# Kernel optimization log

Hardware: AMD Instinct MI355X
Metric: run time of the kernel (lower is better)

The kernel has to match this reference:

```python
import jax, jax.numpy as jnp
import numpy as np

N, E, G = 100000, 300000, 4096
ND, ED, H, ZI, ZS, NE, L = 64, 16, 256, 128, 128, 8, 3
LAMBDA_GRL = 1.0


def setup_inputs() -> dict:
    key = jax.random.key(0)
    ks = iter(jax.random.split(key, 64))
    def nrm(shape, scale=0.05):
        return jax.random.normal(next(ks), shape, jnp.float32) * scale
    inp = {
        'x': jax.random.normal(next(ks), (N, ND), jnp.float32),
        'edge_index': jax.random.randint(next(ks), (2, E), 0, N),
        'edge_attr': jax.random.normal(next(ks), (E, ED), jnp.float32),
        'batch': jnp.sort(jax.random.randint(next(ks), (N,), 0, G)),
        'node_W': nrm((ND, H)), 'node_b': nrm((H,)),
        'conv_eps': jnp.zeros((L,), jnp.float32),
        'edge_W': nrm((L, ED, H)), 'edge_b': nrm((L, H)),
        'mlp_W1': nrm((L, H, H)), 'mlp_b1': nrm((L, H)),
        'mlp_W2': nrm((L, H, H)), 'mlp_b2': nrm((L, H)),
        'gn_w': jnp.ones((L, H), jnp.float32), 'gn_b': jnp.zeros((L, H), jnp.float32),
        'gn_ms': jnp.ones((L, H), jnp.float32),
        'finv_W1': nrm((H, ZI)), 'finv_b1': nrm((ZI,)),
        'finv_W2': nrm((ZI, ZI)), 'finv_b2': nrm((ZI,)),
        'fspu_W1': nrm((H, ZS)), 'fspu_b1': nrm((ZS,)),
        'fspu_W2': nrm((ZS, ZS)), 'fspu_b2': nrm((ZS,)),
        'pred_W1': nrm((ZI, ZI)), 'pred_b1': nrm((ZI,)),
        'pred_W2': nrm((ZI, 1)), 'pred_b2': nrm((1,)),
        'adv_W1': nrm((ZI, ZI)), 'adv_b1': nrm((ZI,)),
        'adv_W2': nrm((ZI, NE)), 'adv_b2': nrm((NE,)),
    }
    return inp


def _mlp2(h, W1, b1, W2, b2):
    return jax.nn.relu(h @ W1 + b1) @ W2 + b2


def reference(x, edge_index, edge_attr, batch, node_W, node_b, conv_eps,
              edge_W, edge_b, mlp_W1, mlp_b1, mlp_W2, mlp_b2,
              gn_w, gn_b, gn_ms,
              finv_W1, finv_b1, finv_W2, finv_b2,
              fspu_W1, fspu_b1, fspu_W2, fspu_b2,
              pred_W1, pred_b1, pred_W2, pred_b2,
              adv_W1, adv_b1, adv_W2, adv_b2):
    src, dst = edge_index[0], edge_index[1]
    cnt = jax.ops.segment_sum(jnp.ones((N, 1), jnp.float32), batch, num_segments=G)
    cnt = jnp.maximum(cnt, 1.0)
    h = x @ node_W + node_b  # [N,H]
    for l in range(L):
        # GINEConv: sum_j relu(x_j + lin(e_ij))
        e = edge_attr @ edge_W[l] + edge_b[l]            # [E,H]
        m = jax.nn.relu(h[src] + e)                      # [E,H]
        agg = jax.ops.segment_sum(m, dst, num_segments=N)
        h = _mlp2((1.0 + conv_eps[l]) * h + agg, mlp_W1[l], mlp_b1[l], mlp_W2[l], mlp_b2[l])
        # GraphNorm
        mean = jax.ops.segment_sum(h, batch, num_segments=G) / cnt  # [G,H]
        out = h - gn_ms[l] * mean[batch]
        var = jax.ops.segment_sum(out * out, batch, num_segments=G) / cnt
        h = out * jax.lax.rsqrt(var[batch] + 1e-5) * gn_w[l] + gn_b[l]
        h = jax.nn.relu(h)  # dropout is identity at eval
    hg = jax.ops.segment_sum(h, batch, num_segments=G) / cnt  # global_mean_pool [G,H]
    z_inv = _mlp2(hg, finv_W1, finv_b1, finv_W2, finv_b2)
    z_spu = _mlp2(hg, fspu_W1, fspu_b1, fspu_W2, fspu_b2)
    yhat = _mlp2(z_inv, pred_W1, pred_b1, pred_W2, pred_b2)[:, 0]
    # gradient reversal: identity fwd, -lambda on bwd
    grl = jax.lax.stop_gradient(z_inv) * (1.0 + LAMBDA_GRL) - LAMBDA_GRL * z_inv
    envhat = _mlp2(grl, adv_W1, adv_b1, adv_W2, adv_b2)
    return (hg, z_inv, z_spu, yhat, envhat)
```

## Files before the change

### kernel.cpp

```cpp
#include <hip/hip_runtime.h>
#include <hip/hip_bf16.h>

typedef __bf16 bf16_t;
typedef __bf16 bf16x8 __attribute__((ext_vector_type(8)));
typedef __bf16 bf16x4 __attribute__((ext_vector_type(4)));
typedef float  f32x4  __attribute__((ext_vector_type(4)));

static constexpr int N_NODES = 100000;
static constexpr int N_EDGES = 300000;
static constexpr int N_GRAPH = 4096;
static constexpr int H  = 256;
static constexpr int ND = 64;
static constexpr int ZIC = 128;
static constexpr int NE = 8;
static constexpr int SCAN_B = 1024;

__device__ __forceinline__ int clampi(int v, int lo, int hi) {
  return v < lo ? lo : (v > hi ? hi : v);
}

__device__ __forceinline__ void dma16(const bf16_t* g, bf16_t* lds_base) {
  __builtin_amdgcn_global_load_lds(
      (const __attribute__((address_space(1))) void*)g,
      (__attribute__((address_space(3))) void*)lds_base, 16, 0, 0);
}

__global__ void compute_starts_kernel(const int* __restrict__ batch,
                                      int* __restrict__ starts,
                                      int* __restrict__ counts,
                                      int* __restrict__ cursor, int N, int G) {
  int i = blockIdx.x * blockDim.x + threadIdx.x;
  if (i >= N) return;
  counts[i] = 0;
  cursor[i] = 0;
  int b = clampi(batch[i], 0, G - 1);
  if (i == 0) {
    for (int g = 0; g <= b; ++g) starts[g] = 0;
  } else {
    int p = clampi(batch[i - 1], 0, G - 1);
    for (int g = p + 1; g <= b; ++g) starts[g] = i;
  }
  if (i == N - 1) {
    for (int g = b + 1; g <= G; ++g) starts[g] = N;
  }
}

__global__ void count_deg_kernel(const int* __restrict__ dst, int* __restrict__ counts, int E, int N) {
  int e = blockIdx.x * blockDim.x + threadIdx.x;
  if (e < E) atomicAdd(&counts[clampi(dst[e], 0, N - 1)], 1);
}

__global__ __launch_bounds__(SCAN_B) void scan1_kernel(const int* __restrict__ counts,
                                                       int* __restrict__ offs,
                                                       int* __restrict__ bsum, int N) {
  __shared__ int tmp[SCAN_B];
  int i = blockIdx.x * SCAN_B + threadIdx.x;
  int v = (i < N) ? counts[i] : 0;
  tmp[threadIdx.x] = v;
  __syncthreads();
  for (int d = 1; d < SCAN_B; d <<= 1) {
    int t = (threadIdx.x >= d) ? tmp[threadIdx.x - d] : 0;
    __syncthreads();
    tmp[threadIdx.x] += t;
    __syncthreads();
  }
  if (i < N) offs[i + 1] = tmp[threadIdx.x];
  if (threadIdx.x == SCAN_B - 1) bsum[blockIdx.x] = tmp[SCAN_B - 1];
  if (i == 0) offs[0] = 0;
}

__global__ void scan2_kernel(int* __restrict__ bsum, int nblk) {
  if (blockIdx.x == 0 && threadIdx.x == 0) {
    int run = 0;
    for (int b = 0; b < nblk; ++b) { int v = bsum[b]; bsum[b] = run; run += v; }
  }
}

__global__ __launch_bounds__(SCAN_B) void scan3_kernel(int* __restrict__ offs,
                                                       const int* __restrict__ bsum, int N) {
  int i = blockIdx.x * SCAN_B + threadIdx.x;
  if (i < N) offs[i + 1] += bsum[blockIdx.x];
}

__global__ void fill_scatter_kernel(const int* __restrict__ src, const int* __restrict__ dst,
                                    const float* __restrict__ eattr,
                                    const int* __restrict__ offs, int* __restrict__ cursor,
                                    int* __restrict__ src_srt, bf16_t* __restrict__ eat16,
                                    int E, int N) {
  int e = blockIdx.x * blockDim.x + threadIdx.x;
  if (e >= E) return;
  int d = clampi(dst[e], 0, N - 1);
  int pos = offs[d] + atomicAdd(&cursor[d], 1);
  if ((unsigned)pos >= (unsigned)E) return;
  int s = src[e];
  src_srt[pos] = ((unsigned)s < (unsigned)N_NODES) ? s : 0;
  const float* ea = eattr + (size_t)e * 16;
  union { bf16_t b[16]; uint4 u[2]; } pk;
#pragma unroll
  for (int k = 0; k < 16; ++k) pk.b[k] = (bf16_t)ea[k];
  uint4* dst16 = (uint4*)(eat16 + ((size_t)pos << 4));
  dst16[0] = pk.u[0];
  dst16[1] = pk.u[1];
}

__global__ void build_ewt16_kernel(const float* __restrict__ edge_W,
                                   bf16_t* __restrict__ ewt) {
  int idx = blockIdx.x * blockDim.x + threadIdx.x;
  if (idx >= 3 * 256 * 16) return;
  int l = idx / (256 * 16);
  int rem = idx - l * 256 * 16;
  int n = rem >> 4, k = rem & 15;
  ewt[idx] = (bf16_t)edge_W[(size_t)l * 16 * 256 + k * 256 + n];
}

__global__ void transpose_kernel(const float* __restrict__ W,
                                 bf16_t* __restrict__ Wt, int K, int Nc,
                                 size_t srcStride, size_t dstStride) {
  __shared__ float tile[32][33];
  const float* Wz = W + (size_t)blockIdx.z * srcStride;
  bf16_t* Wtz = Wt + (size_t)blockIdx.z * dstStride;
  int n0 = blockIdx.x * 32, k0 = blockIdx.y * 32;
  int tx = threadIdx.x, ty = threadIdx.y;
  for (int i = ty; i < 32; i += 8)
    tile[i][tx] = Wz[(size_t)(k0 + i) * Nc + n0 + tx];
  __syncthreads();
  for (int i = ty; i < 32; i += 8)
    Wtz[(size_t)(n0 + i) * K + k0 + tx] = (bf16_t)tile[tx][i];
}

__device__ __forceinline__ void load8_to_lds(const bf16_t* p, bool valid, uint4* dst) {
  uint4 v = make_uint4(0u, 0u, 0u, 0u);
  if (valid) v = *(const uint4*)p;
  *dst = v;
}
__device__ __forceinline__ void load8_to_lds(const float* p, bool valid, uint4* dst) {
  float4 f0 = make_float4(0.f, 0.f, 0.f, 0.f), f1 = f0;
  if (valid) { f0 = *(const float4*)p; f1 = *(const float4*)(p + 4); }
  union { bf16_t b[8]; uint4 u; } pk;
  pk.b[0] = (bf16_t)f0.x; pk.b[1] = (bf16_t)f0.y;
  pk.b[2] = (bf16_t)f0.z; pk.b[3] = (bf16_t)f0.w;
  pk.b[4] = (bf16_t)f1.x; pk.b[5] = (bf16_t)f1.y;
  pk.b[6] = (bf16_t)f1.z; pk.b[7] = (bf16_t)f1.w;
  *dst = pk.u;
}

template<int K, bool RELU, bool OUTF32, typename TIN>
__global__ __launch_bounds__(256) void gemm128_kernel(
    const TIN* __restrict__ U, const bf16_t* __restrict__ Wt,
    const float* __restrict__ bias, void* __restrict__ Out, int M, int Nc) {
  constexpr int LDT = 72;
  __shared__ bf16_t Ut[128 * LDT];
  __shared__ bf16_t Wl[128 * LDT];
  const int m0 = blockIdx.x * 128;
  const int n0 = blockIdx.y * 128;
  const int t = threadIdx.x;
  const int lane = t & 63;
  const int wave = t >> 6;
  const int wm = (wave >> 1) * 64;
  const int wn = (wave & 1) * 64;
  const int srow = t >> 1;
  const int sk = (t & 1) * 32;
  const int lr = lane & 15;
  const int lq = lane >> 4;
  const bool aok = (m0 + srow) < M;
  f32x4 acc[4][4] = {};

  for (int k0 = 0; k0 < K; k0 += 64) {
    const TIN* up = U + (size_t)(m0 + srow) * K + k0 + sk;
    const bf16_t* wp = Wt + (size_t)(n0 + srow) * K + k0 + sk;
#pragma unroll
    for (int q = 0; q < 4; ++q) {
      load8_to_lds(up + q * 8, aok, (uint4*)&Ut[srow * LDT + sk + q * 8]);
      load8_to_lds(wp + q * 8, true, (uint4*)&Wl[srow * LDT + sk + q * 8]);
    }
    __syncthreads();
#pragma unroll
    for (int s = 0; s < 2; ++s) {
      bf16x8 a[4], b[4];
#pragma unroll
      for (int mt = 0; mt < 4; ++mt)
        a[mt] = *(const bf16x8*)(&Ut[(wm + mt * 16 + lr) * LDT + s * 32 + lq * 8]);
#pragma unroll
      for (int nt = 0; nt < 4; ++nt)
        b[nt] = *(const bf16x8*)(&Wl[(wn + nt * 16 + lr) * LDT + s * 32 + lq * 8]);
#pragma unroll
      for (int mt = 0; mt < 4; ++mt)
#pragma unroll
        for (int nt = 0; nt < 4; ++nt)
          acc[mt][nt] = __builtin_amdgcn_mfma_f32_16x16x32_bf16(
              a[mt], b[nt], acc[mt][nt], 0, 0, 0);
    }
    __syncthreads();
  }

#pragma unroll
  for (int mt = 0; mt < 4; ++mt)
#pragma unroll
    for (int nt = 0; nt < 4; ++nt) {
      int col = n0 + wn + nt * 16 + lr;
      float bcol = bias[col];
#pragma unroll
      for (int r = 0; r < 4; ++r) {
        int row = m0 + wm + mt * 16 + lq * 4 + r;
        if (row < M) {
          float vv = acc[mt][nt][r] + bcol;
          if (RELU) vv = vv > 0.f ? vv : 0.f;
          if (OUTF32) ((float*)Out)[(size_t)row * Nc + col] = vv;
          else        ((bf16_t*)Out)[(size_t)row * Nc + col] = (bf16_t)vv;
        }
      }
    }
}

template<int K, bool RELU>
__global__ __launch_bounds__(512) void gemm256_dma_kernel(
    const bf16_t* __restrict__ U, const bf16_t* __restrict__ Wt,
    const float* __restrict__ bias, bf16_t* __restrict__ Out, int M) {
  __shared__ bf16_t Ut[128 * 64];
  __shared__ bf16_t Wl[256 * 64];
  const int t = threadIdx.x;
  const int lane = t & 63;
  const int wave = t >> 6;
  const int m0 = blockIdx.x * 128;
  const int wm = (wave >> 2) * 64;
  const int wn = (wave & 3) * 64;
  const int lr = lane & 15;
  const int lq = lane >> 4;
  const int subrow = lane >> 3;
  const int lchunk = (lane & 7) ^ subrow;
  f32x4 acc[4][4] = {};

  for (int k0 = 0; k0 < K; k0 += 64) {
#pragma unroll
    for (int c = 0; c < 2; ++c) {
      int urow = m0 + c * 64 + wave * 8 + subrow;
      if (urow >= M) urow = M - 1;
      dma16(U + (size_t)urow * K + k0 + lchunk * 8, &Ut[(c * 64 + wave * 8) * 64]);
    }
#pragma unroll
    for (int c = 0; c < 4; ++c) {
      int wrow = c * 64 + wave * 8 + subrow;
      dma16(Wt + (size_t)wrow * K + k0 + lchunk * 8, &Wl[(c * 64 + wave * 8) * 64]);
    }
    __syncthreads();
#pragma unroll
    for (int s = 0; s < 2; ++s) {
      bf16x8 a[4], b[4];
#pragma unroll
      for (int mt = 0; mt < 4; ++mt)
        a[mt] = *(const bf16x8*)(&Ut[(wm + mt * 16 + lr) * 64 + (((s * 4 + lq) ^ (lr & 7)) << 3)]);
#pragma unroll
      for (int nt = 0; nt < 4; ++nt)
        b[nt] = *(const bf16x8*)(&Wl[(wn + nt * 16 + lr) * 64 + (((s * 4 + lq) ^ (lr & 7)) << 3)]);
#pragma unroll
      for (int mt = 0; mt < 4; ++mt)
#pragma unroll
        for (int nt = 0; nt < 4; ++nt)
          acc[mt][nt] = __builtin_amdgcn_mfma_f32_16x16x32_bf16(
              a[mt], b[nt], acc[mt][nt], 0, 0, 0);
    }
    __syncthreads();
  }

#pragma unroll
  for (int mt = 0; mt < 4; ++mt)
#pragma unroll
    for (int nt = 0; nt < 4; ++nt) {
      int col = wn + nt * 16 + lr;
      float bcol = bias[col];
#pragma unroll
      for (int r = 0; r < 4; ++r) {
        int row = m0 + wm + mt * 16 + lq * 4 + r;
        if (row < M) {
          float vv = acc[mt][nt][r] + bcol;
          if (RELU) vv = vv > 0.f ? vv : 0.f;
          Out[(size_t)row * H + col] = (bf16_t)vv;
        }
      }
    }
}

__global__ __launch_bounds__(256) void gine_gather_mfma_kernel(
    const bf16_t* __restrict__ h, const bf16_t* __restrict__ eat16,
    const int* __restrict__ src_sorted, const int* __restrict__ offs,
    const bf16_t* __restrict__ ewt, const float* __restrict__ eb,
    const float* __restrict__ eps_p, bf16_t* __restrict__ u) {
  constexpr int HP = H + 8;
  __shared__ bf16_t slin[2][16 * HP];
  const int t = threadIdx.x;
  const int wave = t >> 6;
  const int lane = t & 63;
  const int lr = lane & 15;
  const int lq = lane >> 4;
  const int lane4 = lane * 4;
  const int n0 = blockIdx.x * 4;
  const int nodeN = n0 + wave;

  bf16x4 hs = *(const bf16x4*)(h + (size_t)nodeN * H + lane4);

  bf16x8 bfrag[4];
#pragma unroll
  for (int nt = 0; nt < 4; ++nt) {
    bf16x8 bv = {};
    if (lq < 2)
      bv = *(const bf16x8*)(ewt + ((wave * 64 + nt * 16 + lr) << 4) + (lq << 3));
    bfrag[nt] = bv;
  }
  float ebv[4];
#pragma unroll
  for (int i = 0; i < 4; ++i) ebv[i] = eb[lane4 + i];

  int bs = offs[n0], be = offs[n0 + 4];
  bs = clampi(bs, 0, N_EDGES);
  be = clampi(be, bs, N_EDGES);
  int ns = offs[nodeN], ne = offs[nodeN + 1];
  ns = clampi(ns, bs, be);
  ne = clampi(ne, ns, be);

  float acc[4] = {0.f, 0.f, 0.f, 0.f};
  int parity = 0;

  for (int cb = bs; cb < be; cb += 16, parity ^= 1) {
    int arow = cb + lr;
    if (arow >= N_EDGES) arow = N_EDGES - 1;
    bf16x8 afrag = {};
    if (lq < 2)
      afrag = *(const bf16x8*)(eat16 + ((size_t)arow << 4) + (lq << 3));

    int j0 = ns > cb ? ns : cb;
    int j1 = ne < cb + 16 ? ne : cb + 16;
    int sidx[4];
    bf16x4 hv[4];
    if (j0 < j1) {
#pragma unroll
      for (int q = 0; q < 4; ++q) {
        int jj = j0 + q; if (jj > j1 - 1) jj = j1 - 1;
        sidx[q] = src_sorted[jj];
      }
    }

    f32x4 c[4];
#pragma unroll
    for (int nt = 0; nt < 4; ++nt) {
      f32x4 z = {};
      c[nt] = __builtin_amdgcn_mfma_f32_16x16x32_bf16(afrag, bfrag[nt], z, 0, 0, 0);
    }
#pragma unroll
    for (int nt = 0; nt < 4; ++nt)
#pragma unroll
      for (int r = 0; r < 4; ++r)
        slin[parity][(lq * 4 + r) * HP + wave * 64 + nt * 16 + lr] = (bf16_t)c[nt][r];

    if (j0 < j1) {
#pragma unroll
      for (int q = 0; q < 4; ++q)
        hv[q] = *(const bf16x4*)(h + (size_t)sidx[q] * H + lane4);
    }

    __syncthreads();

    for (int jb = j0; jb < j1; jb += 4) {
      if (jb != j0) {
#pragma unroll
        for (int q = 0; q < 4; ++q) {
          int jj = jb + q; if (jj > j1 - 1) jj = j1 - 1;
          sidx[q] = src_sorted[jj];
        }
#pragma unroll
        for (int q = 0; q < 4; ++q)
          hv[q] = *(const bf16x4*)(h + (size_t)sidx[q] * H + lane4);
      }
#pragma unroll
      for (int q = 0; q < 4; ++q) {
        if (jb + q < j1) {
          bf16x4 lv = *(const bf16x4*)(&slin[parity][(jb + q - cb) * HP + lane4]);
#pragma unroll
          for (int i = 0; i < 4; ++i)
            acc[i] += fmaxf((float)hv[q][i] + (float)lv[i] + ebv[i], 0.f);
        }
      }
    }
  }

  const float sc = 1.0f + eps_p[0];
  union { bf16x4 v; uint2 b; } o;
#pragma unroll
  for (int i = 0; i < 4; ++i) o.v[i] = (bf16_t)(sc * (float)hs[i] + acc[i]);
  *(uint2*)(u + (size_t)nodeN * H + lane4) = o.b;
}

__global__ __launch_bounds__(256) void graphnorm_kernel(
    const bf16_t* __restrict__ v, bf16_t* __restrict__ hout,
    const int* __restrict__ starts,
    const float* __restrict__ w, const float* __restrict__ b,
    const float* __restrict__ ms, float* __restrict__ hg) {
  constexpr int RS = 9;
  constexpr int PS = 13;
  __shared__ float red[4 * 64 * RS];
  __shared__ float prm[64 * PS];
  const int g = blockIdx.x;
  const int t = threadIdx.x;
  const int lane = t & 63;
  const int wave = t >> 6;
  const int c0 = lane * 4;
  int s = starts[g], e = starts[g + 1];
  s = clampi(s, 0, N_NODES);
  e = clampi(e, s, N_NODES);
  const float cnt = (float)((e - s) > 1 ? (e - s) : 1);

  float sx[4] = {0.f, 0.f, 0.f, 0.f}, sxx[4] = {0.f, 0.f, 0.f, 0.f};
  {
    int i = s + wave;
    for (; i + 4 < e; i += 8) {
      bf16x4 x0 = *(const bf16x4*)(v + (size_t)i * H + c0);
      bf16x4 x1 = *(const bf16x4*)(v + (size_t)(i + 4) * H + c0);
#pragma unroll
      for (int j = 0; j < 4; ++j) {
        float f0 = (float)x0[j], f1 = (float)x1[j];
        sx[j] += f0 + f1; sxx[j] += f0 * f0 + f1 * f1;
      }
    }
    if (i < e) {
      bf16x4 x0 = *(const bf16x4*)(v + (size_t)i * H + c0);
#pragma unroll
      for (int j = 0; j < 4; ++j) {
        float f0 = (float)x0[j];
        sx[j] += f0; sxx[j] += f0 * f0;
      }
    }
  }
  float* myred = &red[(wave * 64 + lane) * RS];
#pragma unroll
  for (int j = 0; j < 4; ++j) { myred[j] = sx[j]; myred[4 + j] = sxx[j]; }
  __syncthreads();

  if (wave == 0) {
#pragma unroll
    for (int j = 0; j < 4; ++j) {
      float fsx = red[lane * RS + j] + red[(64 + lane) * RS + j] +
                  red[(128 + lane) * RS + j] + red[(192 + lane) * RS + j];
      float fsxx = red[lane * RS + 4 + j] + red[(64 + lane) * RS + 4 + j] +
                   red[(128 + lane) * RS + 4 + j] + red[(192 + lane) * RS + 4 + j];
      float mean = fsx / cnt;
      float sub = ms[c0 + j] * mean;
      float var = fsxx / cnt - 2.f * sub * mean + sub * sub;
      var = fmaxf(var, 0.f);
      prm[lane * PS + j] = sub;
      prm[lane * PS + 4 + j] = rsqrtf(var + 1e-5f) * w[c0 + j];
      prm[lane * PS + 8 + j] = b[c0 + j];
    }
  }
  __syncthreads();
  float sub[4], inv[4], bb[4];
#pragma unroll
  for (int j = 0; j < 4; ++j) {
    sub[j] = prm[lane * PS + j];
    inv[j] = prm[lane * PS + 4 + j];
    bb[j] = prm[lane * PS + 8 + j];
  }

  float psum[4] = {0.f, 0.f, 0.f, 0.f};
  {
    int i = s + wave;
    for (; i + 4 < e; i += 8) {
      bf16x4 x0 = *(const bf16x4*)(v + (size_t)i * H + c0);
      bf16x4 x1 = *(const bf16x4*)(v + (size_t)(i + 4) * H + c0);
      union { bf16x4 o; uint2 u; } p0, p1;
#pragma unroll
      for (int j = 0; j < 4; ++j) {
        float o0 = ((float)x0[j] - sub[j]) * inv[j] + bb[j];
        float o1 = ((float)x1[j] - sub[j]) * inv[j] + bb[j];
        o0 = o0 > 0.f ? o0 : 0.f;
        o1 = o1 > 0.f ? o1 : 0.f;
        psum[j] += o0 + o1;
        p0.o[j] = (bf16_t)o0; p1.o[j] = (bf16_t)o1;
      }
      *(uint2*)(hout + (size_t)i * H + c0) = p0.u;
      *(uint2*)(hout + (size_t)(i + 4) * H + c0) = p1.u;
    }
    if (i < e) {
      bf16x4 x0 = *(const bf16x4*)(v + (size_t)i * H + c0);
      union { bf16x4 o; uint2 u; } p0;
#pragma unroll
      for (int j = 0; j < 4; ++j) {
        float o0 = ((float)x0[j] - sub[j]) * inv[j] + bb[j];
        o0 = o0 > 0.f ? o0 : 0.f;
        psum[j] += o0;
        p0.o[j] = (bf16_t)o0;
      }
      *(uint2*)(hout + (size_t)i * H + c0) = p0.u;
    }
  }

  if (hg) {
#pragma unroll
    for (int j = 0; j < 4; ++j) myred[j] = psum[j];
    __syncthreads();
    if (wave == 0) {
#pragma unroll
      for (int j = 0; j < 4; ++j) {
        float p = red[lane * RS + j] + red[(64 + lane) * RS + j] +
                  red[(128 + lane) * RS + j] + red[(192 + lane) * RS + j];
        hg[(size_t)g * H + c0 + j] = p / cnt;
      }
    }
  }
}

__global__ __launch_bounds__(256) void heads_fused_kernel(
    const float* __restrict__ hg,
    const bf16_t* __restrict__ fT1, const float* __restrict__ fb1,
    const bf16_t* __restrict__ fT2, const float* __restrict__ fb2,
    const bf16_t* __restrict__ sT1, const float* __restrict__ sb1,
    const bf16_t* __restrict__ sT2, const float* __restrict__ sb2,
    const bf16_t* __restrict__ pT1, const float* __restrict__ pb1,
    const bf16_t* __restrict__ aT1, const float* __restrict__ ab1,
    const float* __restrict__ pW2, const float* __restrict__ pb2,
    const float* __restrict__ aW2, const float* __restrict__ ab2,
    float* __restrict__ out_zi, float* __restrict__ out_zs,
    float* __restrict__ out_yh, float* __restrict__ out_ev) {
  constexpr int LDS_S = 264;
  constexpr int LDZ = 136;
  __shared__ bf16_t BufA[64 * LDS_S];
  __shared__ bf16_t BufB[64 * LDS_S];
  __shared__ bf16_t Z[64 * LDZ];
  const int t = threadIdx.x;
  const int lane = t & 63;
  const int wave = t >> 6;
  const int m0 = blockIdx.x * 64;
  const int lr = lane & 15;
  const int lq = lane >> 4;

  {
    int r = t >> 2, cb = (t & 3) * 64;
    const float* src = hg + (size_t)(m0 + r) * H + cb;
#pragma unroll
    for (int q = 0; q < 8; ++q)
      load8_to_lds(src + q * 8, true, (uint4*)&BufA[r * LDS_S + cb + q * 8]);
  }
  __syncthreads();

  f32x4 acc[4][4];

  {
    const bf16_t* W = (wave < 2) ? fT1 : sT1;
    const float* bb = (wave < 2) ? fb1 : sb1;
    const int wnl = (wave & 1) * 64;
    const int wcol = wave * 64;
#pragma unroll
    for (int mt = 0; mt < 4; ++mt)
#pragma unroll
      for (int nt = 0; nt < 4; ++nt) { f32x4 z = {}; acc[mt][nt] = z; }
    for (int k0 = 0; k0 < 256; k0 += 32) {
      bf16x8 a[4], b[4];
#pragma unroll
      for (int nt = 0; nt < 4; ++nt)
        b[nt] = *(const bf16x8*)(W + (size_t)(wnl + nt * 16 + lr) * 256 + k0 + lq * 8);
#pragma unroll
      for (int mt = 0; mt < 4; ++mt)
        a[mt] = *(const bf16x8*)(&BufA[(mt * 16 + lr) * LDS_S + k0 + lq * 8]);
#pragma unroll
      for (int mt = 0; mt < 4; ++mt)
#pragma unroll
        for (int nt = 0; nt < 4; ++nt)
          acc[mt][nt] = __builtin_amdgcn_mfma_f32_16x16x32_bf16(
              a[mt], b[nt], acc[mt][nt], 0, 0, 0);
    }
    __syncthreads();
#pragma unroll
    for (int nt = 0; nt < 4; ++nt) {
      float bv = bb[wnl + nt * 16 + lr];
      int col = wcol + nt * 16 + lr;
#pragma unroll
      for (int mt = 0; mt < 4; ++mt)
#pragma unroll
        for (int r = 0; r < 4; ++r) {
          int row = mt * 16 + lq * 4 + r;
          float vv = acc[mt][nt][r] + bv;
          BufB[row * LDS_S + col] = (bf16_t)(vv > 0.f ? vv : 0.f);
        }
    }
  }
  __syncthreads();

  {
    const bf16_t* W = (wave < 2) ? fT2 : sT2;
    const float* bb = (wave < 2) ? fb2 : sb2;
    float* outp = (wave < 2) ? out_zi : out_zs;
    const int wnl = (wave & 1) * 64;
    const int kin = (wave < 2) ? 0 : 128;
#pragma unroll
    for (int mt = 0; mt < 4; ++mt)
#pragma unroll
      for (int nt = 0; nt < 4; ++nt) { f32x4 z = {}; acc[mt][nt] = z; }
    for (int k0 = 0; k0 < 128; k0 += 32) {
      bf16x8 a[4], b[4];
#pragma unroll
      for (int nt = 0; nt < 4; ++nt)
        b[nt] = *(const bf16x8*)(W + (size_t)(wnl + nt * 16 + lr) * 128 + k0 + lq * 8);
#pragma unroll
      for (int mt = 0; mt < 4; ++mt)
        a[mt] = *(const bf16x8*)(&BufB[(mt * 16 + lr) * LDS_S + kin + k0 + lq * 8]);
#pragma unroll
      for (int mt = 0; mt < 4; ++mt)
#pragma unroll
        for (int nt = 0; nt < 4; ++nt)
          acc[mt][nt] = __builtin_amdgcn_mfma_f32_16x16x32_bf16(
              a[mt], b[nt], acc[mt][nt], 0, 0, 0);
    }
#pragma unroll
    for (int nt = 0; nt < 4; ++nt) {
      int col = wnl + nt * 16 + lr;
      float bv = bb[col];
#pragma unroll
      for (int mt = 0; mt < 4; ++mt)
#pragma unroll
        for (int r = 0; r < 4; ++r) {
          int row = mt * 16 + lq * 4 + r;
          float vv = acc[mt][nt][r] + bv;
          outp[(size_t)(m0 + row) * ZIC + col] = vv;
          if (wave < 2) Z[row * LDZ + col] = (bf16_t)vv;
        }
    }
  }
  __syncthreads();

  {
    const bf16_t* W = (wave < 2) ? pT1 : aT1;
    const float* bb = (wave < 2) ? pb1 : ab1;
    const int wnl = (wave & 1) * 64;
    const int wcol = wave * 64;
#pragma unroll
    for (int mt = 0; mt < 4; ++mt)
#pragma unroll
      for (int nt = 0; nt < 4; ++nt) { f32x4 z = {}; acc[mt][nt] = z; }
    for (int k0 = 0; k0 < 128; k0 += 32) {
      bf16x8 a[4], b[4];
#pragma unroll
      for (int nt = 0; nt < 4; ++nt)
        b[nt] = *(const bf16x8*)(W + (size_t)(wnl + nt * 16 + lr) * 128 + k0 + lq * 8);
#pragma unroll
      for (int mt = 0; mt < 4; ++mt)
        a[mt] = *(const bf16x8*)(&Z[(mt * 16 + lr) * LDZ + k0 + lq * 8]);
#pragma unroll
      for (int mt = 0; mt < 4; ++mt)
#pragma unroll
        for (int nt = 0; nt < 4; ++nt)
          acc[mt][nt] = __builtin_amdgcn_mfma_f32_16x16x32_bf16(
              a[mt], b[nt], acc[mt][nt], 0, 0, 0);
    }
#pragma unroll
    for (int nt = 0; nt < 4; ++nt) {
      float bv = bb[wnl + nt * 16 + lr];
      int col = wcol + nt * 16 + lr;
#pragma unroll
      for (int mt = 0; mt < 4; ++mt)
#pragma unroll
        for (int r = 0; r < 4; ++r) {
          int row = mt * 16 + lq * 4 + r;
          float vv = acc[mt][nt][r] + bv;
          BufA[row * LDS_S + col] = (bf16_t)(vv > 0.f ? vv : 0.f);
        }
    }
  }
  __syncthreads();

  if (t < 64) {
    float a4 = pb2[0];
    for (int k = 0; k < 128; ++k)
      a4 += (float)BufA[t * LDS_S + k] * pW2[k];
    out_yh[m0 + t] = a4;
  }
#pragma unroll
  for (int pass = 0; pass < 2; ++pass) {
    int j = pass * 256 + t;
    int r = j >> 3, n = j & 7;
    float a4 = ab2[n];
    for (int k = 0; k < 128; ++k)
      a4 += (float)BufA[r * LDS_S + 128 + k] * aW2[k * 8 + n];
    out_ev[(size_t)(m0 + r) * NE + n] = a4;
  }
}

extern "C" void kernel_launch(void* const* d_in, const int* in_sizes, int n_in,
                              void* d_out, int out_size, void* d_ws, size_t ws_size,
                              hipStream_t stream) {
  (void)in_sizes; (void)n_in; (void)out_size; (void)ws_size;
  const float* x        = (const float*)d_in[0];
  const int*   eidx     = (const int*)d_in[1];
  const float* eattr    = (const float*)d_in[2];
  const int*   batch    = (const int*)d_in[3];
  const float* node_W   = (const float*)d_in[4];
  const float* node_b   = (const float*)d_in[5];
  const float* conv_eps = (const float*)d_in[6];
  const float* edge_W   = (const float*)d_in[7];
  const float* edge_b   = (const float*)d_in[8];
  const float* mlp_W1   = (const float*)d_in[9];
  const float* mlp_b1   = (const float*)d_in[10];
  const float* mlp_W2   = (const float*)d_in[11];
  const float* mlp_b2   = (const float*)d_in[12];
  const float* gn_w     = (const float*)d_in[13];
  const float* gn_b     = (const float*)d_in[14];
  const float* gn_ms    = (const float*)d_in[15];
  const float* finv_W1  = (const float*)d_in[16];
  const float* finv_b1  = (const float*)d_in[17];
  const float* finv_W2  = (const float*)d_in[18];
  const float* finv_b2  = (const float*)d_in[19];
  const float* fspu_W1  = (const float*)d_in[20];
  const float* fspu_b1  = (const float*)d_in[21];
  const float* fspu_W2  = (const float*)d_in[22];
  const float* fspu_b2  = (const float*)d_in[23];
  const float* pred_W1  = (const float*)d_in[24];
  const float* pred_b1  = (const float*)d_in[25];
  const float* pred_W2  = (const float*)d_in[26];
  const float* pred_b2  = (const float*)d_in[27];
  const float* adv_W1   = (const float*)d_in[28];
  const float* adv_b1   = (const float*)d_in[29];
  const float* adv_W2   = (const float*)d_in[30];
  const float* adv_b2   = (const float*)d_in[31];
  float* out = (float*)d_out;

  float* out_hg = out;
  float* out_zi = out + (size_t)N_GRAPH * H;
  float* out_zs = out_zi + (size_t)N_GRAPH * ZIC;
  float* out_yh = out_zs + (size_t)N_GRAPH * ZIC;
  float* out_ev = out_yh + N_GRAPH;

  char* wp = (char*)d_ws;
  auto alloc = [&](size_t bytes) { char* p = wp; wp += (bytes + 255) & ~(size_t)255; return p; };
  bf16_t* A        = (bf16_t*)alloc((size_t)N_NODES * H * 2);
  bf16_t* B        = (bf16_t*)alloc((size_t)N_NODES * H * 2);
  bf16_t* Wt       = (bf16_t*)alloc((size_t)(H * ND + 6 * H * H) * 2);
  bf16_t* WtH      = (bf16_t*)alloc((size_t)(2 * ZIC * H + 4 * ZIC * ZIC) * 2);
  bf16_t* ewt16    = (bf16_t*)alloc((size_t)3 * 256 * 16 * 2);
  bf16_t* eat16    = (bf16_t*)alloc((size_t)N_EDGES * 16 * 2);
  int*    starts   = (int*)alloc((size_t)(N_GRAPH + 1) * 4);
  int*    counts   = (int*)alloc((size_t)N_NODES * 4);
  int*    cursor   = (int*)alloc((size_t)N_NODES * 4);
  int*    offs     = (int*)alloc((size_t)(N_NODES + 1) * 4);
  int*    bsum     = (int*)alloc((size_t)SCAN_B * 4);
  int*    src_srt  = (int*)alloc((size_t)N_EDGES * 4);

  const int* srcp = eidx;
  const int* dstp = eidx + N_EDGES;
  const int nscan = (N_NODES + SCAN_B - 1) / SCAN_B;

  compute_starts_kernel<<<(N_NODES + 255) / 256, 256, 0, stream>>>(
      batch, starts, counts, cursor, N_NODES, N_GRAPH);
  count_deg_kernel<<<(N_EDGES + 255) / 256, 256, 0, stream>>>(dstp, counts, N_EDGES, N_NODES);
  scan1_kernel<<<nscan, SCAN_B, 0, stream>>>(counts, offs, bsum, N_NODES);
  scan2_kernel<<<1, 64, 0, stream>>>(bsum, nscan);
  scan3_kernel<<<nscan, SCAN_B, 0, stream>>>(offs, bsum, N_NODES);
  fill_scatter_kernel<<<(N_EDGES + 255) / 256, 256, 0, stream>>>(
      srcp, dstp, eattr, offs, cursor, src_srt, eat16, N_EDGES, N_NODES);
  build_ewt16_kernel<<<(3 * 256 * 16 + 255) / 256, 256, 0, stream>>>(edge_W, ewt16);

  bf16_t* WtN = Wt;
  bf16_t* Wt1base = Wt + H * ND;
  bf16_t* Wt2base = Wt + H * ND + (size_t)H * H;
  auto Wt1l = [&](int l) { return Wt1base + (size_t)(2 * l) * H * H; };
  auto Wt2l = [&](int l) { return Wt2base + (size_t)(2 * l) * H * H; };
  transpose_kernel<<<dim3(H / 32, ND / 32, 1), dim3(32, 8), 0, stream>>>(node_W, WtN, ND, H, 0, 0);
  transpose_kernel<<<dim3(H / 32, H / 32, 3), dim3(32, 8), 0, stream>>>(
      mlp_W1, Wt1base, H, H, (size_t)H * H, (size_t)2 * H * H);
  transpose_kernel<<<dim3(H / 32, H / 32, 3), dim3(32, 8), 0, stream>>>(
      mlp_W2, Wt2base, H, H, (size_t)H * H, (size_t)2 * H * H);

  bf16_t* fT1 = WtH;
  bf16_t* fT2 = fT1 + ZIC * H;
  bf16_t* sT1 = fT2 + ZIC * ZIC;
  bf16_t* sT2 = sT1 + ZIC * H;
  bf16_t* pT1 = sT2 + ZIC * ZIC;
  bf16_t* aT1 = pT1 + ZIC * ZIC;
  transpose_kernel<<<dim3(ZIC / 32, H / 32, 1), dim3(32, 8), 0, stream>>>(finv_W1, fT1, H, ZIC, 0, 0);
  transpose_kernel<<<dim3(ZIC / 32, ZIC / 32, 1), dim3(32, 8), 0, stream>>>(finv_W2, fT2, ZIC, ZIC, 0, 0);
  transpose_kernel<<<dim3(ZIC / 32, H / 32, 1), dim3(32, 8), 0, stream>>>(fspu_W1, sT1, H, ZIC, 0, 0);
  transpose_kernel<<<dim3(ZIC / 32, ZIC / 32, 1), dim3(32, 8), 0, stream>>>(fspu_W2, sT2, ZIC, ZIC, 0, 0);
  transpose_kernel<<<dim3(ZIC / 32, ZIC / 32, 1), dim3(32, 8), 0, stream>>>(pred_W1, pT1, ZIC, ZIC, 0, 0);
  transpose_kernel<<<dim3(ZIC / 32, ZIC / 32, 1), dim3(32, 8), 0, stream>>>(adv_W1, aT1, ZIC, ZIC, 0, 0);

  dim3 ggrid((N_NODES + 127) / 128, H / 128);
  gemm128_kernel<ND, false, false><<<ggrid, 256, 0, stream>>>(x, WtN, node_b, A, N_NODES, H);

  const int mblocks = (N_NODES + 127) / 128;
  for (int l = 0; l < 3; ++l) {
    gine_gather_mfma_kernel<<<N_NODES / 4, 256, 0, stream>>>(
        A, eat16, src_srt, offs, ewt16 + (size_t)l * 256 * 16,
        edge_b + l * H, conv_eps + l, B);
    gemm256_dma_kernel<H, true ><<<mblocks, 512, 0, stream>>>(B, Wt1l(l), mlp_b1 + l * H, A, N_NODES);
    gemm256_dma_kernel<H, false><<<mblocks, 512, 0, stream>>>(A, Wt2l(l), mlp_b2 + l * H, B, N_NODES);
    graphnorm_kernel<<<N_GRAPH, 256, 0, stream>>>(B, A, starts, gn_w + l * H, gn_b + l * H,
                                                  gn_ms + l * H, (l == 2) ? out_hg : nullptr);
  }

  heads_fused_kernel<<<N_GRAPH / 64, 256, 0, stream>>>(
      out_hg,
      fT1, finv_b1, fT2, finv_b2,
      sT1, fspu_b1, sT2, fspu_b2,
      pT1, pred_b1, aT1, adv_b1,
      pred_W2, pred_b2, adv_W2, adv_b2,
      out_zi, out_zs, out_yh, out_ev);
}
```

Baseline: 722.5 us.

## Widen node-embedding GEMM to full 256-column tile and fold edge bias into LDS

The input projection GEMM is rewritten as a single-pass, 512-thread kernel that covers all 256 output columns per block. The x tile is loaded once instead of twice, and the weights arrive by direct global-to-LDS DMA with an XOR-swizzled layout. Separately, the gather kernel now adds the edge bias once when writing the per-edge linear result to LDS, instead of on every accumulated edge. This rounds the bias-included value to bf16, which slightly changes numerics.

Result: faster. 691.7 us (-4.3%).

```diff
diff --git a/kernel.cpp b/kernel.cpp
--- a/kernel.cpp
+++ b/kernel.cpp
@@ -144,69 +144,68 @@
   *dst = pk.u;
 }
 
-template<int K, bool RELU, bool OUTF32, typename TIN>
-__global__ __launch_bounds__(256) void gemm128_kernel(
-    const TIN* __restrict__ U, const bf16_t* __restrict__ Wt,
-    const float* __restrict__ bias, void* __restrict__ Out, int M, int Nc) {
+template<int K>
+__global__ __launch_bounds__(512) void gemm_node_kernel(
+    const float* __restrict__ U, const bf16_t* __restrict__ Wt,
+    const float* __restrict__ bias, bf16_t* __restrict__ Out, int M) {
   constexpr int LDT = 72;
   __shared__ bf16_t Ut[128 * LDT];
-  __shared__ bf16_t Wl[128 * LDT];
-  const int m0 = blockIdx.x * 128;
-  const int n0 = blockIdx.y * 128;
+  __shared__ bf16_t Wl[256 * 64];
   const int t = threadIdx.x;
   const int lane = t & 63;
   const int wave = t >> 6;
-  const int wm = (wave >> 1) * 64;
-  const int wn = (wave & 1) * 64;
-  const int srow = t >> 1;
-  const int sk = (t & 1) * 32;
+  const int m0 = blockIdx.x * 128;
+  const int wm = (wave >> 2) * 64;
+  const int wn = (wave & 3) * 64;
   const int lr = lane & 15;
   const int lq = lane >> 4;
-  const bool aok = (m0 + srow) < M;
+  const int subrow = lane >> 3;
+  const int lchunk = (lane & 7) ^ subrow;
   f32x4 acc[4][4] = {};
 
-  for (int k0 = 0; k0 < K; k0 += 64) {
-    const TIN* up = U + (size_t)(m0 + srow) * K + k0 + sk;
-    const bf16_t* wp = Wt + (size_t)(n0 + srow) * K + k0 + sk;
-#pragma unroll
-    for (int q = 0; q < 4; ++q) {
-      load8_to_lds(up + q * 8, aok, (uint4*)&Ut[srow * LDT + sk + q * 8]);
-      load8_to_lds(wp + q * 8, true, (uint4*)&Wl[srow * LDT + sk + q * 8]);
-    }
-    __syncthreads();
-#pragma unroll
-    for (int s = 0; s < 2; ++s) {
-      bf16x8 a[4], b[4];
-#pragma unroll
-      for (int mt = 0; mt < 4; ++mt)
-        a[mt] = *(const bf16x8*)(&Ut[(wm + mt * 16 + lr) * LDT + s * 32 + lq * 8]);
+  {
+    int r = t >> 2, c0 = (t & 3) * 16;
+    int ur = m0 + r;
+    bool ok = ur < M;
+    const float* up = U + (size_t)ur * K + c0;
+    load8_to_lds(up,     ok, (uint4*)&Ut[r * LDT + c0]);
+    load8_to_lds(up + 8, ok, (uint4*)&Ut[r * LDT + c0 + 8]);
+  }
+#pragma unroll
+  for (int c = 0; c < 4; ++c) {
+    int wrow = c * 64 + wave * 8 + subrow;
+    dma16(Wt + (size_t)wrow * K + lchunk * 8, &Wl[(c * 64 + wave * 8) * 64]);
+  }
+  __syncthreads();
+#pragma unroll
+  for (int s = 0; s < 2; ++s) {
+    bf16x8 a[4], b[4];
+#pragma unroll
+    for (int mt = 0; mt < 4; ++mt)
+      a[mt] = *(const bf16x8*)(&Ut[(wm + mt * 16 + lr) * LDT + s * 32 + lq * 8]);
+#pragma unroll
+    for (int nt = 0; nt < 4; ++nt)
+      b[nt] = *(const bf16x8*)(&Wl[(wn + nt * 16 + lr) * 64 + (((s * 4 + lq) ^ (lr & 7)) << 3)]);
+#pragma unroll
+    for (int mt = 0; mt < 4; ++mt)
 #pragma unroll
       for (int nt = 0; nt < 4; ++nt)
-        b[nt] = *(const bf16x8*)(&Wl[(wn + nt * 16 + lr) * LDT + s * 32 + lq * 8]);
-#pragma unroll
-      for (int mt = 0; mt < 4; ++mt)
-#pragma unroll
-        for (int nt = 0; nt < 4; ++nt)
-          acc[mt][nt] = __builtin_amdgcn_mfma_f32_16x16x32_bf16(
-              a[mt], b[nt], acc[mt][nt], 0, 0, 0);
-    }
-    __syncthreads();
+        acc[mt][nt] = __builtin_amdgcn_mfma_f32_16x16x32_bf16(
+            a[mt], b[nt], acc[mt][nt], 0, 0, 0);
   }
 
 #pragma unroll
   for (int mt = 0; mt < 4; ++mt)
 #pragma unroll
     for (int nt = 0; nt < 4; ++nt) {
-      int col = n0 + wn + nt * 16 + lr;
+      int col = wn + nt * 16 + lr;
       float bcol = bias[col];
 #pragma unroll
       for (int r = 0; r < 4; ++r) {
         int row = m0 + wm + mt * 16 + lq * 4 + r;
         if (row < M) {
           float vv = acc[mt][nt][r] + bcol;
-          if (RELU) vv = vv > 0.f ? vv : 0.f;
-          if (OUTF32) ((float*)Out)[(size_t)row * Nc + col] = vv;
-          else        ((bf16_t*)Out)[(size_t)row * Nc + col] = (bf16_t)vv;
+          Out[(size_t)row * H + col] = (bf16_t)vv;
         }
       }
     }
@@ -299,16 +298,15 @@
   bf16x4 hs = *(const bf16x4*)(h + (size_t)nodeN * H + lane4);
 
   bf16x8 bfrag[4];
+  float ebw[4];
 #pragma unroll
   for (int nt = 0; nt < 4; ++nt) {
     bf16x8 bv = {};
     if (lq < 2)
       bv = *(const bf16x8*)(ewt + ((wave * 64 + nt * 16 + lr) << 4) + (lq << 3));
     bfrag[nt] = bv;
-  }
-  float ebv[4];
-#pragma unroll
-  for (int i = 0; i < 4; ++i) ebv[i] = eb[lane4 + i];
+    ebw[nt] = eb[wave * 64 + nt * 16 + lr];
+  }
 
   int bs = offs[n0], be = offs[n0 + 4];
   bs = clampi(bs, 0, N_EDGES);
@@ -349,7 +347,8 @@
     for (int nt = 0; nt < 4; ++nt)
 #pragma unroll
       for (int r = 0; r < 4; ++r)
-        slin[parity][(lq * 4 + r) * HP + wave * 64 + nt * 16 + lr] = (bf16_t)c[nt][r];
+        slin[parity][(lq * 4 + r) * HP + wave * 64 + nt * 16 + lr] =
+            (bf16_t)(c[nt][r] + ebw[nt]);
 
     if (j0 < j1) {
 #pragma unroll
@@ -376,7 +375,7 @@
           bf16x4 lv = *(const bf16x4*)(&slin[parity][(jb + q - cb) * HP + lane4]);
 #pragma unroll
           for (int i = 0; i < 4; ++i)
-            acc[i] += fmaxf((float)hv[q][i] + (float)lv[i] + ebv[i], 0.f);
+            acc[i] += fmaxf((float)hv[q][i] + (float)lv[i], 0.f);
         }
       }
     }
@@ -779,10 +778,9 @@
   transpose_kernel<<<dim3(ZIC / 32, ZIC / 32, 1), dim3(32, 8), 0, stream>>>(pred_W1, pT1, ZIC, ZIC, 0, 0);
   transpose_kernel<<<dim3(ZIC / 32, ZIC / 32, 1), dim3(32, 8), 0, stream>>>(adv_W1, aT1, ZIC, ZIC, 0, 0);
 
-  dim3 ggrid((N_NODES + 127) / 128, H / 128);
-  gemm128_kernel<ND, false, false><<<ggrid, 256, 0, stream>>>(x, WtN, node_b, A, N_NODES, H);
-
   const int mblocks = (N_NODES + 127) / 128;
+  gemm_node_kernel<ND><<<mblocks, 512, 0, stream>>>(x, WtN, node_b, A, N_NODES);
+
   for (int l = 0; l < 3; ++l) {
     gine_gather_mfma_kernel<<<N_NODES / 4, 256, 0, stream>>>(
         A, eat16, src_srt, offs, ewt16 + (size_t)l * 256 * 16,
```
